# Kernel optimization log

Measured on AMD Instinct MI355X. Metric: run time of the kernel, lower is better.

## Reference

```python
import jax, jax.numpy as jnp
import numpy as np

B, N, K = 4, 4096, 20
IN_C, OUT_C = 32, 32
EPS = 1e-5


def setup_inputs() -> dict:
    key = jax.random.key(0)
    ks = jax.random.split(key, 10)
    s = 0.05
    return {
        "x": jax.random.normal(ks[0], (B, 3, N), dtype=jnp.float32),
        "feature": jax.random.normal(ks[1], (B, IN_C, N), dtype=jnp.float32),
        "w_mlp": jax.random.normal(ks[2], (IN_C, 7), dtype=jnp.float32) * s,     # Conv1d(7, in_c, 1)
        "b_mlp": jax.random.normal(ks[3], (IN_C,), dtype=jnp.float32) * s,
        "w_att": jax.random.normal(ks[4], (2 * IN_C, 2 * IN_C), dtype=jnp.float32) * s,  # Conv1d(2C,2C,1,bias=False)
        "w_conv": jax.random.normal(ks[5], (OUT_C, 2 * IN_C), dtype=jnp.float32) * s,    # Linear(2C,out_c)
        "b_conv": jax.random.normal(ks[6], (OUT_C,), dtype=jnp.float32) * s,
        "w_out": jax.random.normal(ks[7], (OUT_C, IN_C), dtype=jnp.float32) * s,  # Conv1d(in_c,out_c,1)
        "b_out": jax.random.normal(ks[8], (OUT_C,), dtype=jnp.float32) * s,
        "gamma": jnp.ones((OUT_C,), dtype=jnp.float32),   # BatchNorm1d weight
        "beta": jnp.zeros((OUT_C,), dtype=jnp.float32),   # BatchNorm1d bias
    }


def reference(x, feature, w_mlp, b_mlp, w_att, w_conv, b_conv, w_out, b_out, gamma, beta):
    pts = jnp.swapaxes(x, 1, 2)                       # [B, N, 3]
    # brute-force KNN (argkmin over squared distance); self is nearest (d=0)
    sq = jnp.sum(pts * pts, axis=-1)                  # [B, N]
    d2 = sq[:, :, None] + sq[:, None, :] - 2.0 * jnp.einsum('bnd,bmd->bnm', pts, pts)
    neigh = jax.lax.top_k(-d2, K)[1]                  # [B, N, K] int32

    gather = jax.vmap(lambda v, idx: v[idx])          # per-batch fancy gather
    x_neighs = gather(pts, neigh)                     # [B, N, K, 3]
    x_repeat = jnp.broadcast_to(x_neighs[:, :, 0:1, :], x_neighs.shape)
    x_rel = x_neighs - x_repeat                       # [B, N, K, 3]
    x_dis = jnp.linalg.norm(x_rel, axis=-1, keepdims=True)  # [B, N, K, 1]
    x_feats = jnp.concatenate([x_repeat, x_rel, x_dis], axis=-1)   # [B, N, K, 7]
    x_enc = jnp.einsum('bnkf,cf->bnkc', x_feats, w_mlp) + b_mlp    # [B, N, K, C]

    feat_pts = jnp.swapaxes(feature, 1, 2)            # [B, N, C]
    feat_neighs = gather(feat_pts, neigh)             # [B, N, K, C]
    feats = jnp.concatenate([feat_neighs, x_enc], axis=-1)         # [B, N, K, 2C]

    # attention weights: pointwise conv then softmax over the CHANNEL dim (torch dim=1)
    scores = jnp.einsum('bnkc,dc->bnkd', feats, w_att)             # [B, N, K, 2C]
    attn = jax.nn.softmax(scores, axis=-1)
    pooled = jnp.sum(attn * feats, axis=2)            # sum over neighbors K -> [B, N, 2C]

    out_feat = jnp.einsum('bnc,oc->bno', pooled, w_conv) + b_conv  # [B, N, out_c]
    out_feat = jnp.swapaxes(out_feat, 1, 2)           # [B, out_c, N]
    out_feat = out_feat + jnp.einsum('oc,bcn->bon', w_out, feature) + b_out[None, :, None]

    # BatchNorm1d (training-mode batch statistics over B and N)
    mean = jnp.mean(out_feat, axis=(0, 2), keepdims=True)
    var = jnp.var(out_feat, axis=(0, 2), keepdims=True)
    normed = (out_feat - mean) * jax.lax.rsqrt(var + EPS)
    return normed * gamma[None, :, None] + beta[None, :, None]
```

## Files before the change

kernel.cpp:

```cpp
#include <hip/hip_runtime.h>
#include <hip/hip_bf16.h>

#define BATCH 4
#define NPTS  4096
#define KNBR  20
#define INC   32
#define TWC   64
#define OUTC  32
#define EPSBN 1e-5f

typedef short short8 __attribute__((ext_vector_type(8)));
typedef float f32x16 __attribute__((ext_vector_type(16)));

__device__ __forceinline__ float rlf(float v, int l) {
    return __uint_as_float((unsigned)__builtin_amdgcn_readlane((int)__float_as_uint(v), l));
}
__device__ __forceinline__ ushort f2bf(float x) {
    unsigned u = __float_as_uint(x);
    unsigned r = u + 0x7FFFu + ((u >> 16) & 1u);
    return (ushort)(r >> 16);
}
__device__ __forceinline__ float bf2f(ushort h) {
    return __uint_as_float(((unsigned)h) << 16);
}
__device__ __forceinline__ void gll16(const float4* g, float4* l) {
    __builtin_amdgcn_global_load_lds((const __attribute__((address_space(1))) void*)g,
                                     (__attribute__((address_space(3))) void*)l, 16, 0, 0);
}
__device__ __forceinline__ void barrier_nd() {
    asm volatile("" ::: "memory");
    __builtin_amdgcn_s_barrier();
    asm volatile("" ::: "memory");
}
template <int N> __device__ __forceinline__ void waitVm() {
    if constexpr (N == 0) asm volatile("s_waitcnt vmcnt(0)" ::: "memory");
    else if constexpr (N == 1) asm volatile("s_waitcnt vmcnt(1)" ::: "memory");
    else asm volatile("s_waitcnt vmcnt(2)" ::: "memory");
}

__global__ __launch_bounds__(256) void k_prep(const float* __restrict__ x,
                                              const float* __restrict__ f,
                                              float4* __restrict__ xT4,
                                              ushort* __restrict__ fT,
                                              const float* __restrict__ w_att,
                                              const float* __restrict__ w_conv,
                                              const float* __restrict__ w_out,
                                              const float* __restrict__ w_mlp,
                                              const float* __restrict__ b_mlp,
                                              short8* __restrict__ wattF,
                                              short8* __restrict__ wconvF,
                                              short8* __restrict__ woutF,
                                              float* __restrict__ wmlp8) {
    int i = blockIdx.x * 256 + threadIdx.x;
    if (i < BATCH * NPTS) {
        int b = i / NPTS, n = i % NPTS;
        const float* xb = x + (size_t)b * 3 * NPTS;
        float x0 = xb[n], x1 = xb[NPTS + n], x2 = xb[2 * NPTS + n];
        float sq = fmaf(x2, x2, fmaf(x1, x1, x0 * x0));
        xT4[i] = make_float4(x0, x1, x2, sq);
    }
    if (i < BATCH * INC * NPTS) {
        int n = i % NPTS; int t = i / NPTS; int c = t % INC; int b = t / INC;
        fT[((size_t)(b * NPTS + n)) * INC + c] = f2bf(f[i]);
    }
    if (blockIdx.x == gridDim.x - 1) {
        int t = threadIdx.x;
        for (int idx = t; idx < 14 * 64; idx += 256) {
            int fr = idx >> 6, ln = idx & 63, l31 = ln & 31, h8 = (ln >> 5) * 8;
            short8 v;
            if (fr < 8) {
                int nt = fr >> 2, kt = fr & 3;
                const float* s = w_att + (nt * 32 + l31) * 64 + kt * 16 + h8;
#pragma unroll
                for (int j = 0; j < 8; ++j) v[j] = (short)f2bf(s[j]);
                wattF[fr * 64 + ln] = v;
            } else if (fr < 12) {
                int kt = fr - 8;
                const float* s = w_conv + l31 * 64 + kt * 16 + h8;
#pragma unroll
                for (int j = 0; j < 8; ++j) v[j] = (short)f2bf(s[j]);
                wconvF[kt * 64 + ln] = v;
            } else {
                int kt = fr - 12;
                const float* s = w_out + l31 * 32 + kt * 16 + h8;
#pragma unroll
                for (int j = 0; j < 8; ++j) v[j] = (short)f2bf(s[j]);
                woutF[kt * 64 + ln] = v;
            }
        }
        for (int idx = t; idx < 512; idx += 256) {
            int e = idx >> 3, j = idx & 7;
            wmlp8[idx] = (j < 7) ? w_mlp[e * 7 + j] : b_mlp[e];
        }
    }
}

#define CAP   192
#define PPBK  8
#define FWSZ  (KNBR * 64)
__global__ __launch_bounds__(512, 6) void k_fused(const float4* __restrict__ xT4,
                                                  const ushort* __restrict__ fbT,
                                                  const float* __restrict__ wmlp8,
                                                  const short8* __restrict__ wattF,
                                                  const short8* __restrict__ wconvF,
                                                  const short8* __restrict__ woutF,
                                                  float* __restrict__ out) {
    __shared__ __align__(16) char smA[36864];
    float4*             candB = (float4*)smA;
    unsigned long long* survB = (unsigned long long*)(smA + 24576);
    ushort*             FbB   = (ushort*)smA;
    __shared__ int scnt[PPBK], slot[PPBK];
    __shared__ int neighL[PPBK][KNBR];
    __shared__ __align__(16) ushort pool[PPBK][64];

    const int tid  = threadIdx.x;
    const int lane = tid & 63;
    const int wv   = tid >> 6;
    const int hi   = lane >> 5;
    const int l31  = lane & 31;
    const int gp   = blockIdx.x * PPBK + wv;
    const int b    = gp >> 12;
    const int nb   = gp & (NPTS - 1);
    const float4* base = xT4 + (size_t)b * NPTS;

    if (lane == 0) { scnt[wv] = 0; slot[wv] = 1; }

    float4 me = xT4[gp];
    asm volatile("s_waitcnt vmcnt(0)" ::: "memory");

    auto stage = [&](int c) {
        const float4* src = base + c * 512 + wv * 64 + lane;
        float4* dst = candB + (c % 3) * 512 + wv * 64;
        gll16(src, dst);
    };
    auto dist = [&](const float4& o) -> unsigned {
        float dot = fmaf(o.z, me.z, fmaf(o.y, me.y, o.x * me.x));
        return __float_as_uint(fmaxf((me.w + o.w) - 2.0f * dot, 0.0f));
    };

    stage(0); stage(1); stage(2);

    unsigned bits[16];
    unsigned lmin = 0xFFFFFFFFu, lmin2 = 0xFFFFFFFFu;

    waitVm<2>(); barrier_nd();
#pragma unroll
    for (int j = 0; j < 8; ++j) {
        unsigned bb = dist(candB[lane + 64 * j]);
        bits[j] = bb;
        unsigned lo_ = bb < lmin ? bb : lmin;
        unsigned hi_ = bb < lmin ? lmin : bb;
        lmin = lo_;
        lmin2 = hi_ < lmin2 ? hi_ : lmin2;
    }
    barrier_nd(); stage(3);

    waitVm<2>(); barrier_nd();
#pragma unroll
    for (int j = 0; j < 8; ++j) {
        unsigned bb = dist(candB[512 + lane + 64 * j]);
        bits[8 + j] = bb;
        unsigned lo_ = bb < lmin ? bb : lmin;
        unsigned hi_ = bb < lmin ? lmin : bb;
        lmin = lo_;
        lmin2 = hi_ < lmin2 ? hi_ : lmin2;
    }
    barrier_nd(); stage(4);

    unsigned lo = 0u, hi2 = 0xFF000000u;
    for (int it = 0; it < 16 && lo < hi2; ++it) {
        unsigned mid = lo + ((hi2 - lo) >> 1);
        int c = __popcll(__ballot(lmin <= mid)) + __popcll(__ballot(lmin2 <= mid));
        if (c >= KNBR) hi2 = mid; else lo = mid + 1;
    }
    const unsigned tau = hi2;

#pragma unroll
    for (int j = 0; j < 16; ++j) {
        if (bits[j] <= tau) {
            int pos = atomicAdd(&scnt[wv], 1);
            if (pos < CAP)
                survB[wv * CAP + pos] = ((unsigned long long)bits[j] << 32) | (unsigned)(lane + 64 * j);
        }
    }

#pragma unroll
    for (int ch = 2; ch < 8; ++ch) {
        if (ch <= 5) waitVm<2>(); else if (ch == 6) waitVm<1>(); else waitVm<0>();
        barrier_nd();
        const float4* cb = candB + (ch % 3) * 512;
        const int ib = ch * 512 + lane;
#pragma unroll
        for (int j = 0; j < 8; ++j) {
            unsigned bb = dist(cb[lane + 64 * j]);
            if (bb <= tau) {
                int pos = atomicAdd(&scnt[wv], 1);
                if (pos < CAP)
                    survB[wv * CAP + pos] = ((unsigned long long)bb << 32) | (unsigned)(ib + 64 * j);
            }
        }
        barrier_nd();
        if (ch < 5) stage(ch + 3);
    }

    int cnt = scnt[wv]; if (cnt > CAP) cnt = CAP;
    const unsigned long long* sv = survB + wv * CAP;

    if (cnt <= 128) {
        unsigned long long k0 = (lane      < cnt) ? sv[lane     ] : ~0ull;
        unsigned long long k1 = (lane + 64 < cnt) ? sv[lane + 64] : ~0ull;
        unsigned d0 = (unsigned)(k0 >> 32), d1 = (unsigned)(k1 >> 32);
        unsigned i0 = (unsigned)k0, i1 = (unsigned)k1;

        unsigned th;
        {
            unsigned l2 = 0u, h2 = tau;
            bool found = false;
            for (int it = 0; it < 32; ++it) {
                unsigned mid = l2 + ((h2 - l2) >> 1);
                int c = __popcll(__ballot(d0 <= mid)) + __popcll(__ballot(d1 <= mid));
                if (c >= KNBR) h2 = mid; else l2 = mid + 1;
                if (c == KNBR) {
                    unsigned mm = (d0 <= mid) ? d0 : 0u;
                    unsigned m2_ = (d1 <= mid) ? d1 : 0u;
                    mm = mm > m2_ ? mm : m2_;
#pragma unroll
                    for (int off = 32; off >= 1; off >>= 1) {
                        unsigned o = __shfl_xor(mm, off, 64);
                        mm = o > mm ? o : mm;
                    }
                    th = mm; found = true; break;
                }
                if (l2 >= h2) break;
            }
            if (!found) th = h2;
        }
        int cless = __popcll(__ballot(d0 < th)) + __popcll(__ballot(d1 < th));
        int need = KNBR - cless;
        bool t0 = (d0 == th), t1 = (d1 == th);
        int tcnt = __popcll(__ballot(t0)) + __popcll(__ballot(t1));
        unsigned idxthr = 0xFFFFFFFFu;
        if (tcnt != need) {
            unsigned la = 0u, ha = 0xFFFFFFFFu;
            for (int it = 0; it < 32; ++it) {
                unsigned mid = la + ((ha - la) >> 1);
                int c = __popcll(__ballot(t0 && i0 <= mid)) + __popcll(__ballot(t1 && i1 <= mid));
                if (c >= need) ha = mid; else la = mid + 1;
            }
            idxthr = ha;
        }
        bool s0 = (d0 < th) || (t0 && i0 <= idxthr);
        bool s1 = (d1 < th) || (t1 && i1 <= idxthr);

        unsigned long long mk = k0 < k1 ? k0 : k1;
#pragma unroll
        for (int off = 32; off >= 1; off >>= 1) {
            unsigned long long o = __shfl_xor(mk, off, 64);
            mk = o < mk ? o : mk;
        }
        if (s0) { if (k0 == mk) neighL[wv][0] = (int)i0; else { int p = atomicAdd(&slot[wv], 1); neighL[wv][p] = (int)i0; } }
        if (s1) { if (k1 == mk) neighL[wv][0] = (int)i1; else { int p = atomicAdd(&slot[wv], 1); neighL[wv][p] = (int)i1; } }
    } else {
        unsigned long long k0 = (lane       < cnt) ? sv[lane      ] : ~0ull;
        unsigned long long k1 = (lane +  64 < cnt) ? sv[lane +  64] : ~0ull;
        unsigned long long k2 = (lane + 128 < cnt) ? sv[lane + 128] : ~0ull;
        unsigned d0 = (unsigned)(k0 >> 32), d1 = (unsigned)(k1 >> 32), d2 = (unsigned)(k2 >> 32);
        unsigned i0 = (unsigned)k0, i1 = (unsigned)k1, i2 = (unsigned)k2;

        unsigned l2 = 0u, h2 = tau;
        for (int it = 0; it < 32 && l2 < h2; ++it) {
            unsigned mid = l2 + ((h2 - l2) >> 1);
            int c = __popcll(__ballot(d0 <= mid)) + __popcll(__ballot(d1 <= mid))
                  + __popcll(__ballot(d2 <= mid));
            if (c >= KNBR) h2 = mid; else l2 = mid + 1;
        }
        const unsigned th = h2;
        int cless = __popcll(__ballot(d0 < th)) + __popcll(__ballot(d1 < th))
                  + __popcll(__ballot(d2 < th));
        int need = KNBR - cless;
        bool t0 = (d0 == th), t1 = (d1 == th), t2 = (d2 == th);
        int tcnt = __popcll(__ballot(t0)) + __popcll(__ballot(t1)) + __popcll(__ballot(t2));
        unsigned idxthr = 0xFFFFFFFFu;
        if (tcnt != need) {
            unsigned la = 0u, ha = 0xFFFFFFFFu;
            for (int it = 0; it < 32; ++it) {
                unsigned mid = la + ((ha - la) >> 1);
                int c = __popcll(__ballot(t0 && i0 <= mid)) + __popcll(__ballot(t1 && i1 <= mid))
                      + __popcll(__ballot(t2 && i2 <= mid));
                if (c >= need) ha = mid; else la = mid + 1;
            }
            idxthr = ha;
        }
        bool s0 = (d0 < th) || (t0 && i0 <= idxthr);
        bool s1 = (d1 < th) || (t1 && i1 <= idxthr);
        bool s2 = (d2 < th) || (t2 && i2 <= idxthr);

        unsigned long long m01 = k0 < k1 ? k0 : k1;
        unsigned long long mk  = m01 < k2 ? m01 : k2;
#pragma unroll
        for (int off = 32; off >= 1; off >>= 1) {
            unsigned long long o = __shfl_xor(mk, off, 64);
            mk = o < mk ? o : mk;
        }
        if (s0) { if (k0 == mk) neighL[wv][0] = (int)i0; else { int p = atomicAdd(&slot[wv], 1); neighL[wv][p] = (int)i0; } }
        if (s1) { if (k1 == mk) neighL[wv][0] = (int)i1; else { int p = atomicAdd(&slot[wv], 1); neighL[wv][p] = (int)i1; } }
        if (s2) { if (k2 == mk) neighL[wv][0] = (int)i2; else { int p = atomicAdd(&slot[wv], 1); neighL[wv][p] = (int)i2; } }
    }

    __syncthreads();

    const ushort* fb = fbT + (size_t)b * NPTS * INC;
    ushort* Fw = FbB + wv * FWSZ;

    int nv = 0;
    if (l31 < KNBR) nv = neighL[wv][l31];
    float4 ncl = base[nv];

    float wm[8];
    {
        const float4* w8 = (const float4*)(wmlp8 + l31 * 8);
        float4 a = w8[0], bq = w8[1];
        wm[0] = a.x; wm[1] = a.y; wm[2] = a.z; wm[3] = a.w;
        wm[4] = bq.x; wm[5] = bq.y; wm[6] = bq.z; wm[7] = bq.w;
    }
    const float c0x = rlf(ncl.x, 0), c0y = rlf(ncl.y, 0), c0z = rlf(ncl.z, 0);

    ushort fr[KNBR];
#pragma unroll
    for (int k = 0; k < KNBR; ++k) {
        int snk = __builtin_amdgcn_readlane(nv, k);
        fr[k] = fb[(size_t)snk * INC + l31];
    }

    float rxl = ncl.x - c0x, ryl = ncl.y - c0y, rzl = ncl.z - c0z;
    float disl = sqrtf(fmaf(rzl, rzl, fmaf(ryl, ryl, rxl * rxl)));

    float fmbase = wm[7];
    fmbase = fmaf(wm[0], c0x, fmbase); fmbase = fmaf(wm[1], c0y, fmbase);
    fmbase = fmaf(wm[2], c0z, fmbase);
#pragma unroll
    for (int k = 0; k < KNBR; ++k) {
        float fm = fmbase;
        fm = fmaf(wm[3], rlf(rxl, k), fm);
        fm = fmaf(wm[4], rlf(ryl, k), fm);
        fm = fmaf(wm[5], rlf(rzl, k), fm);
        fm = fmaf(wm[6], rlf(disl, k), fm);
        ushort fbits = hi ? f2bf(fm) : fr[k];
        Fw[k * 64 + (lane ^ ((k & 7) << 3))] = fbits;
    }

    const int rowA = (l31 < KNBR) ? l31 : (KNBR - 1);
    short8 Af[4];
#pragma unroll
    for (int kt = 0; kt < 4; ++kt) {
        int c0 = kt * 16 + 8 * hi;
        Af[kt] = *(const short8*)&Fw[rowA * 64 + (c0 ^ ((rowA & 7) << 3))];
    }

    float mloc, zloc;
    {
        f32x16 af;
#pragma unroll
        for (int i = 0; i < 16; ++i) af[i] = 0.f;
        __builtin_amdgcn_s_setprio(1);
#pragma unroll
        for (int kt = 0; kt < 4; ++kt)
            af = __builtin_amdgcn_mfma_f32_32x32x16_bf16(wattF[kt * 64 + lane], Af[kt], af, 0, 0, 0);
        __builtin_amdgcn_s_setprio(0);
        float m0 = af[0];
#pragma unroll
        for (int i = 1; i < 16; ++i) m0 = fmaxf(m0, af[i]);
        float z0 = 0.f;
#pragma unroll
        for (int i = 0; i < 16; ++i) z0 += __expf(af[i] - m0);
        mloc = m0; zloc = z0;
    }
    {
        f32x16 af;
#pragma unroll
        for (int i = 0; i < 16; ++i) af[i] = 0.f;
        __builtin_amdgcn_s_setprio(1);
#pragma unroll
        for (int kt = 0; kt < 4; ++kt)
            af = __builtin_amdgcn_mfma_f32_32x32x16_bf16(wattF[(4 + kt) * 64 + lane], Af[kt], af, 0, 0, 0);
        __builtin_amdgcn_s_setprio(0);
        float m1 = af[0];
#pragma unroll
        for (int i = 1; i < 16; ++i) m1 = fmaxf(m1, af[i]);
        float z1 = 0.f;
#pragma unroll
        for (int i = 0; i < 16; ++i) z1 += __expf(af[i] - m1);
        float mn = fmaxf(mloc, m1);
        zloc = zloc * __expf(mloc - mn) + z1 * __expf(m1 - mn);
        mloc = mn;
    }
    float mo = fmaxf(mloc, __shfl_xor(mloc, 32, 64));
    float zs = zloc * __expf(mloc - mo);
    float Zk = zs + __shfl_xor(zs, 32, 64);
    float mzl = mo + __logf(Zk);

    float pooled0 = 0.f, pooled1 = 0.f;
    {
        f32x16 acc;
#pragma unroll
        for (int i = 0; i < 16; ++i) acc[i] = 0.f;
        __builtin_amdgcn_s_setprio(1);
#pragma unroll
        for (int kt = 0; kt < 4; ++kt)
            acc = __builtin_amdgcn_mfma_f32_32x32x16_bf16(Af[kt], wattF[kt * 64 + lane], acc, 0, 0, 0);
        __builtin_amdgcn_s_setprio(0);
#pragma unroll
        for (int r = 0; r < 12; ++r) {
            int j = (r & 3) + 8 * (r >> 2) + 4 * hi;
            float a0 = __expf(acc[r] - rlf(mzl, j));
            float f0 = bf2f(Fw[j * 64 + (l31 ^ ((j & 7) << 3))]);
            float p0 = a0 * f0;
            if (r >= 8) p0 = hi ? 0.f : p0;
            pooled0 += p0;
        }
    }
    {
        f32x16 acc;
#pragma unroll
        for (int i = 0; i < 16; ++i) acc[i] = 0.f;
        __builtin_amdgcn_s_setprio(1);
#pragma unroll
        for (int kt = 0; kt < 4; ++kt)
            acc = __builtin_amdgcn_mfma_f32_32x32x16_bf16(Af[kt], wattF[(4 + kt) * 64 + lane], acc, 0, 0, 0);
        __builtin_amdgcn_s_setprio(0);
#pragma unroll
        for (int r = 0; r < 12; ++r) {
            int j = (r & 3) + 8 * (r >> 2) + 4 * hi;
            float a1 = __expf(acc[r] - rlf(mzl, j));
            float f1 = bf2f(Fw[j * 64 + ((32 + l31) ^ ((j & 7) << 3))]);
            float p1 = a1 * f1;
            if (r >= 8) p1 = hi ? 0.f : p1;
            pooled1 += p1;
        }
    }
    pooled0 += __shfl_xor(pooled0, 32, 64);
    pooled1 += __shfl_xor(pooled1, 32, 64);
    if (!hi) {
        pool[wv][l31]      = f2bf(pooled0);
        pool[wv][32 + l31] = f2bf(pooled1);
    }

    f32x16 oa;
#pragma unroll
    for (int i = 0; i < 16; ++i) oa[i] = 0.f;
    __builtin_amdgcn_s_setprio(1);
#pragma unroll
    for (int kt = 0; kt < 4; ++kt) {
        short8 bb = *(const short8*)&pool[wv][kt * 16 + 8 * hi];
        oa = __builtin_amdgcn_mfma_f32_32x32x16_bf16(wconvF[kt * 64 + lane], bb, oa, 0, 0, 0);
    }
#pragma unroll
    for (int kt = 0; kt < 2; ++kt) {
        short8 bb = *(const short8*)(fb + (size_t)nb * INC + kt * 16 + 8 * hi);
        oa = __builtin_amdgcn_mfma_f32_32x32x16_bf16(woutF[kt * 64 + lane], bb, oa, 0, 0, 0);
    }
    __builtin_amdgcn_s_setprio(0);
#pragma unroll
    for (int r = 0; r < 16; ++r) {
        int o = (r & 3) + 8 * (r >> 2) + 4 * hi;
        if (l31 == 0) out[((size_t)(b * OUTC + o)) * NPTS + nb] = oa[r];
    }
}

__global__ __launch_bounds__(256) void k_bn(float* __restrict__ of,
                                            const float* __restrict__ gamma,
                                            const float* __restrict__ beta) {
    const int c = blockIdx.x;
    const int tid = threadIdx.x;
    float s = 0.f, s2 = 0.f;
#pragma unroll
    for (int b = 0; b < BATCH; ++b) {
        const float4* p = (const float4*)(of + ((size_t)b * OUTC + c) * NPTS);
        for (int i = tid; i < NPTS / 4; i += 256) {
            float4 v = p[i];
            s += (v.x + v.y) + (v.z + v.w);
            s2 = fmaf(v.x, v.x, s2); s2 = fmaf(v.y, v.y, s2);
            s2 = fmaf(v.z, v.z, s2); s2 = fmaf(v.w, v.w, s2);
        }
    }
#pragma unroll
    for (int off = 32; off >= 1; off >>= 1) {
        s += __shfl_xor(s, off, 64);
        s2 += __shfl_xor(s2, off, 64);
    }
    __shared__ float rs[4], rs2[4];
    __shared__ float sc[2];
    if ((tid & 63) == 0) { rs[tid >> 6] = s; rs2[tid >> 6] = s2; }
    __syncthreads();
    if (tid == 0) {
        float S = (rs[0] + rs[1]) + (rs[2] + rs[3]);
        float S2 = (rs2[0] + rs2[1]) + (rs2[2] + rs2[3]);
        const float invn = 1.0f / (BATCH * NPTS);
        float mean = S * invn;
        float var = S2 * invn - mean * mean;
        float rstd = rsqrtf(var + EPSBN);
        float scale = rstd * gamma[c];
        sc[0] = scale;
        sc[1] = beta[c] - mean * scale;
    }
    __syncthreads();
    const float scale = sc[0], shift = sc[1];
#pragma unroll
    for (int b = 0; b < BATCH; ++b) {
        float4* p = (float4*)(of + ((size_t)b * OUTC + c) * NPTS);
        for (int i = tid; i < NPTS / 4; i += 256) {
            float4 v = p[i];
            v.x = fmaf(v.x, scale, shift);
            v.y = fmaf(v.y, scale, shift);
            v.z = fmaf(v.z, scale, shift);
            v.w = fmaf(v.w, scale, shift);
            p[i] = v;
        }
    }
}

extern "C" void kernel_launch(void* const* d_in, const int* in_sizes, int n_in,
                              void* d_out, int out_size, void* d_ws, size_t ws_size,
                              hipStream_t stream) {
    const float* x      = (const float*)d_in[0];
    const float* feat   = (const float*)d_in[1];
    const float* w_mlp  = (const float*)d_in[2];
    const float* b_mlp  = (const float*)d_in[3];
    const float* w_att  = (const float*)d_in[4];
    const float* w_conv = (const float*)d_in[5];
    const float* w_out  = (const float*)d_in[7];
    const float* gamma  = (const float*)d_in[9];
    const float* beta   = (const float*)d_in[10];
    float* out = (float*)d_out;

    char* ws = (char*)d_ws;
    float4* xT4    = (float4*)ws;
    ushort* fbT    = (ushort*)(ws + 262144);
    short8* wattF  = (short8*)(ws + 1310976);
    short8* wconvF = (short8*)(ws + 1319168);
    short8* woutF  = (short8*)(ws + 1323264);
    float*  wmlp8  = (float*)(ws + 1325312);

    k_prep<<<(BATCH * INC * NPTS + 255) / 256 + 1, 256, 0, stream>>>(
        x, feat, xT4, fbT, w_att, w_conv, w_out, w_mlp, b_mlp,
        wattF, wconvF, woutF, wmlp8);
    k_fused<<<(BATCH * NPTS) / PPBK, 512, 0, stream>>>(xT4, fbT, wmlp8,
                                                       wattF, wconvF, woutF, out);
    k_bn<<<OUTC, 256, 0, stream>>>(out, gamma, beta);
}
```

Baseline: 84.49 us.

## Prefilter KNN candidates by x-coordinate distance and switch to double-buffered staging

Adds a separate x-coordinate array so each candidate is first tested with a cheap 1D squared-difference bound against the threshold, and the full float4 distance read is skipped when that test fails. Staging goes from triple to double buffering with an extra 4-byte global-to-LDS load per chunk, which also shrinks shared memory. The bound is padded with a small slack to guard against rounding. Risks: more load instructions per stage, less prefetch depth, and the float4 LDS reads are only avoided when whole wavefronts skip, which makes the benefit data dependent.

```diff
diff --git a/kernel.cpp b/kernel.cpp
--- a/kernel.cpp
+++ b/kernel.cpp
@@ -27,6 +27,10 @@
     __builtin_amdgcn_global_load_lds((const __attribute__((address_space(1))) void*)g,
                                      (__attribute__((address_space(3))) void*)l, 16, 0, 0);
 }
+__device__ __forceinline__ void gll4(const float* g, float* l) {
+    __builtin_amdgcn_global_load_lds((const __attribute__((address_space(1))) void*)g,
+                                     (__attribute__((address_space(3))) void*)l, 4, 0, 0);
+}
 __device__ __forceinline__ void barrier_nd() {
     asm volatile("" ::: "memory");
     __builtin_amdgcn_s_barrier();
@@ -41,6 +45,7 @@
 __global__ __launch_bounds__(256) void k_prep(const float* __restrict__ x,
                                               const float* __restrict__ f,
                                               float4* __restrict__ xT4,
+                                              float* __restrict__ xsT,
                                               ushort* __restrict__ fT,
                                               const float* __restrict__ w_att,
                                               const float* __restrict__ w_conv,
@@ -58,6 +63,7 @@
         float x0 = xb[n], x1 = xb[NPTS + n], x2 = xb[2 * NPTS + n];
         float sq = fmaf(x2, x2, fmaf(x1, x1, x0 * x0));
         xT4[i] = make_float4(x0, x1, x2, sq);
+        xsT[i] = x0;
     }
     if (i < BATCH * INC * NPTS) {
         int n = i % NPTS; int t = i / NPTS; int c = t % INC; int b = t / INC;
@@ -99,15 +105,17 @@
 #define PPBK  8
 #define FWSZ  (KNBR * 64)
 __global__ __launch_bounds__(512, 6) void k_fused(const float4* __restrict__ xT4,
+                                                  const float* __restrict__ xsT,
                                                   const ushort* __restrict__ fbT,
                                                   const float* __restrict__ wmlp8,
                                                   const short8* __restrict__ wattF,
                                                   const short8* __restrict__ wconvF,
                                                   const short8* __restrict__ woutF,
                                                   float* __restrict__ out) {
-    __shared__ __align__(16) char smA[36864];
+    __shared__ __align__(16) char smA[32768];
     float4*             candB = (float4*)smA;
-    unsigned long long* survB = (unsigned long long*)(smA + 24576);
+    float*              xsB   = (float*)(smA + 16384);
+    unsigned long long* survB = (unsigned long long*)(smA + 20480);
     ushort*             FbB   = (ushort*)smA;
     __shared__ int scnt[PPBK], slot[PPBK];
     __shared__ int neighL[PPBK][KNBR];
@@ -122,6 +130,7 @@
     const int b    = gp >> 12;
     const int nb   = gp & (NPTS - 1);
     const float4* base = xT4 + (size_t)b * NPTS;
+    const float*  xsrc = xsT + (size_t)b * NPTS;
 
     if (lane == 0) { scnt[wv] = 0; slot[wv] = 1; }
 
@@ -129,16 +138,16 @@
     asm volatile("s_waitcnt vmcnt(0)" ::: "memory");
 
     auto stage = [&](int c) {
-        const float4* src = base + c * 512 + wv * 64 + lane;
-        float4* dst = candB + (c % 3) * 512 + wv * 64;
-        gll16(src, dst);
+        int off = c * 512 + wv * 64 + lane;
+        gll16(base + off, candB + (c & 1) * 512 + wv * 64);
+        gll4(xsrc + off, xsB + (c & 1) * 512 + wv * 64);
     };
     auto dist = [&](const float4& o) -> unsigned {
         float dot = fmaf(o.z, me.z, fmaf(o.y, me.y, o.x * me.x));
         return __float_as_uint(fmaxf((me.w + o.w) - 2.0f * dot, 0.0f));
     };
 
-    stage(0); stage(1); stage(2);
+    stage(0); stage(1);
 
     unsigned bits[16];
     unsigned lmin = 0xFFFFFFFFu, lmin2 = 0xFFFFFFFFu;
@@ -153,7 +162,7 @@
         lmin = lo_;
         lmin2 = hi_ < lmin2 ? hi_ : lmin2;
     }
-    barrier_nd(); stage(3);
+    barrier_nd(); stage(2);
 
     waitVm<2>(); barrier_nd();
 #pragma unroll
@@ -165,7 +174,7 @@
         lmin = lo_;
         lmin2 = hi_ < lmin2 ? hi_ : lmin2;
     }
-    barrier_nd(); stage(4);
+    barrier_nd(); stage(3);
 
     unsigned lo = 0u, hi2 = 0xFF000000u;
     for (int it = 0; it < 16 && lo < hi2; ++it) {
@@ -174,6 +183,8 @@
         if (c >= KNBR) hi2 = mid; else lo = mid + 1;
     }
     const unsigned tau = hi2;
+    const float mex = me.x;
+    const float thrx = fmaf(__uint_as_float(tau), 1.00001f, 2.0e-4f);
 
 #pragma unroll
     for (int j = 0; j < 16; ++j) {
@@ -186,21 +197,25 @@
 
 #pragma unroll
     for (int ch = 2; ch < 8; ++ch) {
-        if (ch <= 5) waitVm<2>(); else if (ch == 6) waitVm<1>(); else waitVm<0>();
+        if (ch < 7) waitVm<2>(); else waitVm<0>();
         barrier_nd();
-        const float4* cb = candB + (ch % 3) * 512;
+        const float4* cb = candB + (ch & 1) * 512;
+        const float*  xb2 = xsB + (ch & 1) * 512;
         const int ib = ch * 512 + lane;
 #pragma unroll
         for (int j = 0; j < 8; ++j) {
-            unsigned bb = dist(cb[lane + 64 * j]);
-            if (bb <= tau) {
-                int pos = atomicAdd(&scnt[wv], 1);
-                if (pos < CAP)
-                    survB[wv * CAP + pos] = ((unsigned long long)bb << 32) | (unsigned)(ib + 64 * j);
+            float dx = xb2[lane + 64 * j] - mex;
+            if (dx * dx <= thrx) {
+                unsigned bb = dist(cb[lane + 64 * j]);
+                if (bb <= tau) {
+                    int pos = atomicAdd(&scnt[wv], 1);
+                    if (pos < CAP)
+                        survB[wv * CAP + pos] = ((unsigned long long)bb << 32) | (unsigned)(ib + 64 * j);
+                }
             }
         }
         barrier_nd();
-        if (ch < 5) stage(ch + 3);
+        if (ch < 6) stage(ch + 2);
     }
 
     int cnt = scnt[wv]; if (cnt > CAP) cnt = CAP;
@@ -540,11 +555,12 @@
     short8* wconvF = (short8*)(ws + 1319168);
     short8* woutF  = (short8*)(ws + 1323264);
     float*  wmlp8  = (float*)(ws + 1325312);
+    float*  xsT    = (float*)(ws + 1327360);
 
     k_prep<<<(BATCH * INC * NPTS + 255) / 256 + 1, 256, 0, stream>>>(
-        x, feat, xT4, fbT, w_att, w_conv, w_out, w_mlp, b_mlp,
+        x, feat, xT4, xsT, fbT, w_att, w_conv, w_out, w_mlp, b_mlp,
         wattF, wconvF, woutF, wmlp8);
-    k_fused<<<(BATCH * NPTS) / PPBK, 512, 0, stream>>>(xT4, fbT, wmlp8,
+    k_fused<<<(BATCH * NPTS) / PPBK, 512, 0, stream>>>(xT4, xsT, fbT, wmlp8,
                                                        wattF, wconvF, woutF, out);
     k_bn<<<OUTC, 256, 0, stream>>>(out, gamma, beta);
 }
```

New measurement: 91.36 us. 8.1% more time.
